# Kernel tuning notes

Hardware: AMD Instinct MI355X
Metric: run time of the kernel (lower is better)

The kernel has to match this reference:

```python
import jax, jax.numpy as jnp
import numpy as np

B, S, D, H = 2, 2048, 256, 8

def setup_inputs() -> dict:
    key = jax.random.key(0)
    ks = jax.random.split(key, 7)
    inputs = jax.random.normal(ks[0], (B, S, D), dtype=jnp.float32)
    timestamp = jnp.sort(jax.random.randint(ks[1], (B, S), 0, 100000, dtype=jnp.int32), axis=-1)
    wQ = jax.random.normal(ks[2], (H, D, D), dtype=jnp.float32) * 0.05
    wK = jax.random.normal(ks[3], (H, D, D), dtype=jnp.float32) * 0.05
    wV = jax.random.normal(ks[4], (H, D, D), dtype=jnp.float32) * 0.05
    wO = jax.random.normal(ks[5], (H * D, D), dtype=jnp.float32) * 0.05
    theta = jax.random.uniform(ks[6], (1, 1), dtype=jnp.float32)
    return {"inputs": inputs, "timestamp": timestamp, "wQ": wQ, "wK": wK,
            "wV": wV, "wO": wO, "theta": theta}

def reference(inputs, timestamp, wQ, wK, wV, wO, theta):
    b, s, d = inputs.shape
    # per-head projections (original loops over heads via TensorArray; vectorized here)
    Q = jnp.einsum('bsd,hde->bhse', inputs, wQ)
    K = jnp.einsum('bsd,hde->bhse', inputs, wK)
    V = jnp.einsum('bsd,hde->bhse', inputs, wV)
    exp_x = jnp.einsum('bhsd,bhtd->bhst', Q, K) / jnp.sqrt(jnp.float32(d))  # [B,H,S,S]
    x = jax.nn.softmax(exp_x, axis=-1)
    low_tri = jnp.tril(jnp.ones((s, s), dtype=jnp.float32))
    x = x * low_tri
    x = x / jnp.sum(x, axis=-1, keepdims=True)  # causal renormalized softmax

    # time-decay double-softmax branch. NOTE: the original module computes `a`
    # but returns x @ V, so `a`/`s_`/`d_` do not affect the output (dead code,
    # reproduced here for fidelity; XLA will DCE it).
    ts = timestamp.astype(jnp.float32)
    d_t = ts[:, None, :, None] - ts[:, None, None, :]  # diag(t) - t : [B,1,S,S]
    decay = (1.0 - jnp.cumsum(x, axis=-1)) * d_t * low_tri
    s_ = exp_x * jnp.exp(-(theta[0, 0] * theta[0, 0]) * decay)
    a = jax.nn.softmax(s_, axis=-1) * low_tri
    a = a / jnp.sum(a, axis=-1, keepdims=True)
    del a  # unused in original output

    ret = jnp.einsum('bhst,bhtd->bhsd', x, V)          # [B,H,S,D]
    out = ret.transpose(0, 2, 1, 3).reshape(b, s, -1)  # concat heads -> [B,S,H*D]
    return out @ wO
```

## Files before the change

kernel.cpp:

```cpp
#include <hip/hip_runtime.h>
#include <cstdint>
#include <cstddef>

#define S_LEN 2048
#define DIM   256
#define NH    8
#define NB    2
#define HDIM  (NH * DIM)

using bf16 = __bf16;
typedef __bf16 bf16x8 __attribute__((ext_vector_type(8)));
typedef __bf16 bf16x4 __attribute__((ext_vector_type(4)));
typedef float  f32x4  __attribute__((ext_vector_type(4)));


__global__ __launch_bounds__(256) void cast_x_kernel(const float* __restrict__ in,
                                                     bf16* __restrict__ out) {
    int i = (blockIdx.x * 256 + threadIdx.x) * 4;
    float4 v = *(const float4*)(in + i);
    bf16x4 o;
    o[0] = (bf16)v.x; o[1] = (bf16)v.y; o[2] = (bf16)v.z; o[3] = (bf16)v.w;
    *(bf16x4*)(out + i) = o;
}

__global__ __launch_bounds__(256) void transpose_cast_kernel(const float* __restrict__ in,
                                                             bf16* __restrict__ out,
                                                             int R, int C) {
    __shared__ float tile[64][65];
    const size_t msz = (size_t)R * C;
    in  += (size_t)blockIdx.z * msz;
    out += (size_t)blockIdx.z * msz;
    const int c0 = blockIdx.x * 64, r0 = blockIdx.y * 64;
    const int tr  = threadIdx.x >> 4;
    const int tc4 = (threadIdx.x & 15) * 4;
    #pragma unroll
    for (int p = 0; p < 4; ++p) {
        int row = p * 16 + tr;
        float4 v = *(const float4*)(in + (size_t)(r0 + row) * C + c0 + tc4);
        tile[row][tc4+0] = v.x; tile[row][tc4+1] = v.y;
        tile[row][tc4+2] = v.z; tile[row][tc4+3] = v.w;
    }
    __syncthreads();
    #pragma unroll
    for (int p = 0; p < 4; ++p) {
        int orow = p * 16 + tr;
        bf16x4 o;
        #pragma unroll
        for (int j = 0; j < 4; ++j) o[j] = (bf16)tile[tc4 + j][orow];
        *(bf16x4*)(out + (size_t)(c0 + orow) * R + r0 + tc4) = o;
    }
}

template<int EPI>
__device__ __forceinline__ void gemm_tile(const bf16* __restrict__ A, const bf16* __restrict__ BT,
                                          void* __restrict__ C, bf16* As, bf16* Bs,
                                          int tm, int tn, int K, int lda, int ldb, int ldc)
{
    const int tid  = threadIdx.x;
    const int lane = tid & 63;
    const int wave = tid >> 6;
    const int wm   = (wave >> 1) << 6;
    const int wn   = (wave & 1) << 6;
    const int l16  = lane & 15;
    const int quad = lane >> 4;

    const int m0 = tm << 7, n0 = tn << 7;

    f32x4 acc[4][4] = {};

    const int ksteps = K >> 5;
    for (int ks = 0; ks < ksteps; ++ks) {
        const int k0 = ks << 5;
        #pragma unroll
        for (int i = 0; i < 2; ++i) {
            int c = tid + (i << 8);
            int row = c >> 2, off = (c & 3) << 3;
            *(uint4*)(As + row*40 + off) = *(const uint4*)(A  + (size_t)(m0 + row)*lda + k0 + off);
            *(uint4*)(Bs + row*40 + off) = *(const uint4*)(BT + (size_t)(n0 + row)*ldb + k0 + off);
        }
        __syncthreads();
        bf16x8 af[4], bfv[4];
        #pragma unroll
        for (int i = 0; i < 4; ++i) af[i]  = *(const bf16x8*)(As + (wm + i*16 + l16)*40 + quad*8);
        #pragma unroll
        for (int i = 0; i < 4; ++i) bfv[i] = *(const bf16x8*)(Bs + (wn + i*16 + l16)*40 + quad*8);
        #pragma unroll
        for (int i = 0; i < 4; ++i)
            #pragma unroll
            for (int j = 0; j < 4; ++j)
                acc[i][j] = __builtin_amdgcn_mfma_f32_16x16x32_bf16(af[i], bfv[j], acc[i][j], 0, 0, 0);
        __syncthreads();
    }

    #pragma unroll
    for (int i = 0; i < 4; ++i)
        #pragma unroll
        for (int j = 0; j < 4; ++j)
            #pragma unroll
            for (int r = 0; r < 4; ++r) {
                int mg = m0 + wm + i*16 + quad*4 + r;
                int ng = n0 + wn + j*16 + l16;
                float v = acc[i][j][r];
                if (EPI == 0)      ((bf16*)C)[(size_t)mg * ldc + ng] = (bf16)v;
                else if (EPI == 1) ((float*)C)[(size_t)mg * ldc + ng] = v;
                else               atomicAdd(&((float*)C)[(size_t)mg * ldc + ng], v);
            }
}

__global__ __launch_bounds__(256) void proj_kernel(const bf16* __restrict__ Xb,
    const bf16* __restrict__ WQt, const bf16* __restrict__ WKt, const bf16* __restrict__ WVt,
    bf16* __restrict__ Qg, bf16* __restrict__ Kg, bf16* __restrict__ VTg)
{
    __shared__ __align__(16) bf16 smem[2 * 128 * 40];
    const int by  = blockIdx.y;
    const int mat = by >> 4;
    const int b   = (by >> 3) & 1;
    const int h   = by & 7;
    const int bx  = blockIdx.x;
    const bf16*  Xbb = Xb + (size_t)b * S_LEN * DIM;
    const size_t bh  = (size_t)(b * NH + h);
    if (mat == 0) {
        gemm_tile<0>(Xbb, WQt + (size_t)h*DIM*DIM, Qg + bh*S_LEN*DIM, smem, smem + 128*40,
                     bx & 15, bx >> 4, DIM, DIM, DIM, DIM);
    } else if (mat == 1) {
        gemm_tile<0>(Xbb, WKt + (size_t)h*DIM*DIM, Kg + bh*S_LEN*DIM, smem, smem + 128*40,
                     bx & 15, bx >> 4, DIM, DIM, DIM, DIM);
    } else {
        gemm_tile<0>(WVt + (size_t)h*DIM*DIM, Xbb, VTg + bh*DIM*S_LEN, smem, smem + 128*40,
                     bx & 1, bx >> 1, DIM, DIM, DIM, S_LEN);
    }
}

__global__ __launch_bounds__(256) void outproj_kernel(const bf16* __restrict__ Ret,
                                                      const bf16* __restrict__ WOt,
                                                      float* __restrict__ out)
{
    __shared__ __align__(16) bf16 smem[2 * 128 * 40];
    int bx = blockIdx.x;
    int t  = bx & 63;
    int kq = bx >> 6;
    gemm_tile<2>(Ret + kq*512, WOt + kq*512, out, smem, smem + 128*40,
                 t >> 1, t & 1, 512, HDIM, HDIM, DIM);
}

__global__ __launch_bounds__(256) void attn_kernel(const bf16* __restrict__ Qg,
                                                   const bf16* __restrict__ Kg,
                                                   const bf16* __restrict__ VTg,
                                                   bf16* __restrict__ Ret,
                                                   bf16* __restrict__ Opart,
                                                   float* __restrict__ Lpart)
{
    __shared__ __align__(16) bf16 Ks [32 * 264];
    __shared__ __align__(16) bf16 VTs[256 * 40];
    __shared__ __align__(16) bf16 Ps [4 * 16 * 40];

    const int tid  = threadIdx.x;
    const int lane = tid & 63;
    const int wave = tid >> 6;
    const int l16  = lane & 15;
    const int quad = lane >> 4;

    const int bx = blockIdx.x;
    const int R  = (bx < 256) ? bx : (bx < 512 ? 767 - bx : bx);
    const int bh = R & 15;
    const int r  = R >> 4;
    int qt, s; bool split;
    if (r < 40) {
        const int g = r / 5, j = r % 5;
        if (j == 0)      { qt = 15 - g;     split = false; s = 0; }
        else if (j <= 2) { qt = 31 - 2*g;   split = true;  s = j - 1; }
        else             { qt = 30 - 2*g;   split = true;  s = j - 3; }
    } else { qt = 47 - r; split = false; s = 0; }
    const int b = bh >> 3, h = bh & 7;

    int kstep0, kstep1;
    if (split) { kstep0 = s * (qt + 1); kstep1 = kstep0 + qt + 1; }
    else       { kstep0 = 0;           kstep1 = 2*qt + 2; }

    const bf16* Qbh  = Qg  + (size_t)(b*NH + h) * S_LEN * DIM;
    const bf16* Kbh  = Kg  + (size_t)(b*NH + h) * S_LEN * DIM;
    const bf16* VTbh = VTg + (size_t)(b*NH + h) * DIM * S_LEN;

    const int qbase = qt * 64 + wave * 16;

    bf16x8 qf[8];
    #pragma unroll
    for (int kc = 0; kc < 8; ++kc)
        qf[kc] = *(const bf16x8*)(Qbh + (size_t)(qbase + l16)*DIM + kc*32 + quad*8);

    f32x4 o[16] = {};
    float l_part[4] = {0.f, 0.f, 0.f, 0.f};

    for (int step = kstep0; step < kstep1; ++step) {
        const int t0 = step << 5;
        #pragma unroll
        for (int i = 0; i < 4; ++i) {
            int c = tid + (i << 8);
            int row = c >> 5, off = (c & 31) << 3;
            *(uint4*)(Ks + row*264 + off) = *(const uint4*)(Kbh + (size_t)(t0 + row)*DIM + off);
        }
        #pragma unroll
        for (int i = 0; i < 4; ++i) {
            int c = tid + (i << 8);
            int row = c >> 2, off = (c & 3) << 3;
            *(uint4*)(VTs + row*40 + off) = *(const uint4*)(VTbh + (size_t)row*S_LEN + t0 + off);
        }
        __syncthreads();

        f32x4 sacc[2] = {};
        #pragma unroll
        for (int kc = 0; kc < 8; ++kc) {
            bf16x8 b0 = *(const bf16x8*)(Ks + (l16)*264      + kc*32 + quad*8);
            bf16x8 b1 = *(const bf16x8*)(Ks + (16 + l16)*264 + kc*32 + quad*8);
            sacc[0] = __builtin_amdgcn_mfma_f32_16x16x32_bf16(qf[kc], b0, sacc[0], 0,0,0);
            sacc[1] = __builtin_amdgcn_mfma_f32_16x16x32_bf16(qf[kc], b1, sacc[1], 0,0,0);
        }

        float pv[2][4];
        #pragma unroll
        for (int r2 = 0; r2 < 4; ++r2) {
            const int qgi = qbase + quad*4 + r2;
            const bool ok0 = (t0 + l16)      <= qgi;
            const bool ok1 = (t0 + 16 + l16) <= qgi;
            float p0 = ok0 ? __expf(sacc[0][r2] * 0.0625f) : 0.0f;
            float p1 = ok1 ? __expf(sacc[1][r2] * 0.0625f) : 0.0f;
            l_part[r2] += p0 + p1;
            pv[0][r2] = p0; pv[1][r2] = p1;
        }

        #pragma unroll
        for (int nt = 0; nt < 2; ++nt)
            #pragma unroll
            for (int r2 = 0; r2 < 4; ++r2)
                Ps[wave*640 + (quad*4 + r2)*40 + nt*16 + l16] = (bf16)pv[nt][r2];
        __syncthreads();

        bf16x8 pf = *(const bf16x8*)(Ps + wave*640 + l16*40 + quad*8);
        #pragma unroll
        for (int ct = 0; ct < 16; ++ct) {
            bf16x8 vf = *(const bf16x8*)(VTs + (ct*16 + l16)*40 + quad*8);
            o[ct] = __builtin_amdgcn_mfma_f32_16x16x32_bf16(pf, vf, o[ct], 0,0,0);
        }
        __syncthreads();
    }

    float lsum[4];
    #pragma unroll
    for (int r2 = 0; r2 < 4; ++r2) {
        float l = l_part[r2];
        l += __shfl_xor(l, 1);
        l += __shfl_xor(l, 2);
        l += __shfl_xor(l, 4);
        l += __shfl_xor(l, 8);
        lsum[r2] = l;
    }

    if (!split) {
        #pragma unroll
        for (int r2 = 0; r2 < 4; ++r2) {
            const int qgi = qbase + quad*4 + r2;
            const float inv = 1.0f / lsum[r2];
            #pragma unroll
            for (int ct = 0; ct < 16; ++ct)
                Ret[((size_t)b*S_LEN + qgi)*HDIM + h*DIM + ct*16 + l16] = (bf16)(o[ct][r2] * inv);
        }
    } else {
        const size_t slot = ((size_t)(bh*16 + (qt - 16)))*2 + s;
        bf16*  Ob = Opart + slot * (64*256);
        float* Lb = Lpart + slot * 64;
        #pragma unroll
        for (int r2 = 0; r2 < 4; ++r2) {
            const int trow = wave*16 + quad*4 + r2;
            #pragma unroll
            for (int ct = 0; ct < 16; ++ct)
                Ob[(size_t)trow*256 + ct*16 + l16] = (bf16)o[ct][r2];
            if (l16 == 0) Lb[trow] = lsum[r2];
        }
    }
}

__global__ __launch_bounds__(256) void combine_kernel(const bf16* __restrict__ Opart,
                                                      const float* __restrict__ Lpart,
                                                      bf16* __restrict__ Ret)
{
    const int bx  = blockIdx.x;
    const int bh  = bx >> 4;
    const int qti = bx & 15;
    const int b = bh >> 3, h = bh & 7;
    const int row  = threadIdx.x >> 2;
    const int col0 = (threadIdx.x & 3) * 64;

    const size_t slot0 = ((size_t)(bh*16 + qti))*2;
    const bf16* O0 = Opart + slot0 * (64*256) + (size_t)row*256 + col0;
    const bf16* O1 = O0 + 64*256;
    const float inv = 1.0f / (Lpart[slot0*64 + row] + Lpart[(slot0+1)*64 + row]);

    const int q = (qti + 16)*64 + row;
    bf16* dst = Ret + ((size_t)b*S_LEN + q)*HDIM + h*DIM + col0;
    #pragma unroll
    for (int ch = 0; ch < 8; ++ch) {
        bf16x8 a = *(const bf16x8*)(O0 + ch*8);
        bf16x8 c = *(const bf16x8*)(O1 + ch*8);
        bf16x8 w;
        #pragma unroll
        for (int j = 0; j < 8; ++j) w[j] = (bf16)(((float)a[j] + (float)c[j]) * inv);
        *(bf16x8*)(dst + ch*8) = w;
    }
}


extern "C" void kernel_launch(void* const* d_in, const int* in_sizes, int n_in,
                              void* d_out, int out_size, void* d_ws, size_t ws_size,
                              hipStream_t stream)
{
    (void)in_sizes; (void)n_in; (void)ws_size;
    const float* X  = (const float*)d_in[0];
    const float* wQ = (const float*)d_in[2];
    const float* wK = (const float*)d_in[3];
    const float* wV = (const float*)d_in[4];
    const float* wO = (const float*)d_in[5];

    char* ws = (char*)d_ws;
    const size_t MB = 1u << 20;
    bf16*  Xb    = (bf16*)(ws + 0*MB);
    bf16*  WQt   = (bf16*)(ws + 2*MB);
    bf16*  WKt   = (bf16*)(ws + 3*MB);
    bf16*  WVt   = (bf16*)(ws + 4*MB);
    bf16*  WOt   = (bf16*)(ws + 5*MB);
    bf16*  Qg    = (bf16*)(ws + 6*MB);
    bf16*  Kg    = (bf16*)(ws + 22*MB);
    bf16*  VTg   = (bf16*)(ws + 38*MB);
    bf16*  Ret   = (bf16*)(ws + 54*MB);
    bf16*  Opart = (bf16*)(ws + 70*MB);
    float* Lpart = (float*)(ws + 86*MB);

    hipMemsetAsync(d_out, 0, (size_t)out_size * sizeof(float), stream);

    cast_x_kernel        <<<1024, 256, 0, stream>>>(X, Xb);
    transpose_cast_kernel<<<dim3(4, 4, 8),  256, 0, stream>>>(wQ, WQt, DIM, DIM);
    transpose_cast_kernel<<<dim3(4, 4, 8),  256, 0, stream>>>(wK, WKt, DIM, DIM);
    transpose_cast_kernel<<<dim3(4, 4, 8),  256, 0, stream>>>(wV, WVt, DIM, DIM);
    transpose_cast_kernel<<<dim3(4, 32, 1), 256, 0, stream>>>(wO, WOt, HDIM, DIM);
    proj_kernel    <<<dim3(32, 48), 256, 0, stream>>>(Xb, WQt, WKt, WVt, Qg, Kg, VTg);
    attn_kernel    <<<768,          256, 0, stream>>>(Qg, Kg, VTg, Ret, Opart, Lpart);
    combine_kernel <<<256,          256, 0, stream>>>(Opart, Lpart, Ret);
    outproj_kernel <<<256,          256, 0, stream>>>(Ret, WOt, (float*)d_out);
}
```

Before: 229.7 us.

## Double-buffer attention K/V tiles with async global-to-LDS loads and XOR swizzle

Replaces the synchronous register-staged K and V^T tile loads in the attention kernel with global_load_lds direct-to-LDS copies into two ping-pong buffers. The next step's tiles are prefetched while the current step computes. Padded LDS rows are replaced by XOR-swizzled unpadded layouts to avoid bank conflicts. This doubles LDS use for K/V and relies on vmcnt waits plus a barrier per step for correctness.

```diff
diff --git a/kernel.cpp b/kernel.cpp
--- a/kernel.cpp
+++ b/kernel.cpp
@@ -12,6 +12,13 @@
 typedef __bf16 bf16x8 __attribute__((ext_vector_type(8)));
 typedef __bf16 bf16x4 __attribute__((ext_vector_type(4)));
 typedef float  f32x4  __attribute__((ext_vector_type(4)));
+
+typedef const __attribute__((address_space(1))) unsigned int* as1_u32p;
+typedef __attribute__((address_space(3))) unsigned int* as3_u32p;
+
+__device__ __forceinline__ void cp16(const bf16* g, bf16* l) {
+    __builtin_amdgcn_global_load_lds((as1_u32p)g, (as3_u32p)l, 16, 0, 0);
+}
 
 
 __global__ __launch_bounds__(256) void cast_x_kernel(const float* __restrict__ in,
@@ -143,6 +150,27 @@
                  t >> 1, t & 1, 512, HDIM, HDIM, DIM);
 }
 
+__device__ __forceinline__ void stage_tiles(const bf16* __restrict__ Kbh,
+                                            const bf16* __restrict__ VTbh,
+                                            bf16* Ksbuf, bf16* Vsbuf,
+                                            int t0, int wave, int lane)
+{
+    #pragma unroll
+    for (int j = 0; j < 4; ++j) {
+        const int s  = (((wave << 2) + j) << 6) + lane;
+        const int ts = s >> 5, cs = s & 31;
+        cp16(Kbh + (size_t)(t0 + ts)*DIM + ((cs ^ ts) << 3),
+             Ksbuf + (((wave << 2) + j) << 9));
+    }
+    #pragma unroll
+    for (int j = 0; j < 4; ++j) {
+        const int s  = (((wave << 2) + j) << 6) + lane;
+        const int es = s >> 2, cs = s & 3;
+        cp16(VTbh + (size_t)es*S_LEN + t0 + ((cs ^ ((es >> 1) & 3)) << 3),
+             Vsbuf + (((wave << 2) + j) << 9));
+    }
+}
+
 __global__ __launch_bounds__(256) void attn_kernel(const bf16* __restrict__ Qg,
                                                    const bf16* __restrict__ Kg,
                                                    const bf16* __restrict__ VTg,
@@ -150,9 +178,9 @@
                                                    bf16* __restrict__ Opart,
                                                    float* __restrict__ Lpart)
 {
-    __shared__ __align__(16) bf16 Ks [32 * 264];
-    __shared__ __align__(16) bf16 VTs[256 * 40];
-    __shared__ __align__(16) bf16 Ps [4 * 16 * 40];
+    __shared__ __align__(16) bf16 KsB [2][32 * 256];
+    __shared__ __align__(16) bf16 VTsB[2][256 * 32];
+    __shared__ __align__(16) bf16 Ps  [4 * 16 * 40];
 
     const int tid  = threadIdx.x;
     const int lane = tid & 63;
@@ -191,27 +219,26 @@
     f32x4 o[16] = {};
     float l_part[4] = {0.f, 0.f, 0.f, 0.f};
 
+    stage_tiles(Kbh, VTbh, &KsB[0][0], &VTsB[0][0], kstep0 << 5, wave, lane);
+
     for (int step = kstep0; step < kstep1; ++step) {
+        const int pb = (step - kstep0) & 1;
+        asm volatile("s_waitcnt vmcnt(0)" ::: "memory");
+        __syncthreads();
+        if (step + 1 < kstep1)
+            stage_tiles(Kbh, VTbh, &KsB[pb ^ 1][0], &VTsB[pb ^ 1][0],
+                        (step + 1) << 5, wave, lane);
+
         const int t0 = step << 5;
-        #pragma unroll
-        for (int i = 0; i < 4; ++i) {
-            int c = tid + (i << 8);
-            int row = c >> 5, off = (c & 31) << 3;
-            *(uint4*)(Ks + row*264 + off) = *(const uint4*)(Kbh + (size_t)(t0 + row)*DIM + off);
-        }
-        #pragma unroll
-        for (int i = 0; i < 4; ++i) {
-            int c = tid + (i << 8);
-            int row = c >> 2, off = (c & 3) << 3;
-            *(uint4*)(VTs + row*40 + off) = *(const uint4*)(VTbh + (size_t)row*S_LEN + t0 + off);
-        }
-        __syncthreads();
+        const bf16* KsP = &KsB[pb][0];
+        const bf16* VsP = &VTsB[pb][0];
 
         f32x4 sacc[2] = {};
         #pragma unroll
         for (int kc = 0; kc < 8; ++kc) {
-            bf16x8 b0 = *(const bf16x8*)(Ks + (l16)*264      + kc*32 + quad*8);
-            bf16x8 b1 = *(const bf16x8*)(Ks + (16 + l16)*264 + kc*32 + quad*8);
+            const int ch = (kc << 2) + quad;
+            bf16x8 b0 = *(const bf16x8*)(KsP + (l16 << 8)        + ((ch ^ l16) << 3));
+            bf16x8 b1 = *(const bf16x8*)(KsP + ((16 + l16) << 8) + ((ch ^ (16 + l16)) << 3));
             sacc[0] = __builtin_amdgcn_mfma_f32_16x16x32_bf16(qf[kc], b0, sacc[0], 0,0,0);
             sacc[1] = __builtin_amdgcn_mfma_f32_16x16x32_bf16(qf[kc], b1, sacc[1], 0,0,0);
         }
@@ -238,10 +265,10 @@
         bf16x8 pf = *(const bf16x8*)(Ps + wave*640 + l16*40 + quad*8);
         #pragma unroll
         for (int ct = 0; ct < 16; ++ct) {
-            bf16x8 vf = *(const bf16x8*)(VTs + (ct*16 + l16)*40 + quad*8);
+            const int e = (ct << 4) + l16;
+            bf16x8 vf = *(const bf16x8*)(VsP + (e << 5) + ((quad ^ ((e >> 1) & 3)) << 3));
             o[ct] = __builtin_amdgcn_mfma_f32_16x16x32_bf16(pf, vf, o[ct], 0,0,0);
         }
-        __syncthreads();
     }
 
     float lsum[4];
```

Result: faster. 216.3 us (-5.8%).
